# Kernel optimization log

Measured on AMD Instinct MI355X. Metric: run time of the kernel, lower is better.

Reference implementation:

```python
import jax, jax.numpy as jnp
import numpy as np

EPS = 1e-12  # matches tf l2_normalize epsilon behavior closely enough for testing

def setup_inputs() -> dict:
    key = jax.random.key(0)
    k1, k2 = jax.random.split(key)
    B, M, D = 512, 65536, 512
    context = jax.random.normal(k1, (B, D), dtype=jnp.float32)
    memory = jax.random.normal(k2, (M, D), dtype=jnp.float32)
    return {"context": context, "memory": memory}

def reference(context, memory):
    # tf.keras.losses.cosine_similarity returns NEGATIVE cosine similarity:
    # sim[b,m] = -sum(l2norm(context[b]) * l2norm(memory[m]))
    ctx_n = context / jnp.sqrt(jnp.maximum(jnp.sum(context * context, axis=-1, keepdims=True), EPS))
    mem_n = memory / jnp.sqrt(jnp.maximum(jnp.sum(memory * memory, axis=-1, keepdims=True), EPS))
    sim = -jnp.einsum('bd,md->bm', ctx_n, mem_n)  # [B, M]
    best = jnp.argmin(sim, axis=-1)               # [B], = argmax cosine
    # recall: gather then expand_dims(axis=0) -> [1, B, D]
    return memory[best][None, :, :]
```

## Files before the change

### kernel.cpp

```cpp
#include <hip/hip_runtime.h>
#include <hip/hip_bf16.h>
#include <stdint.h>

#define D_DIM 512
#define B_CTX 512
#define M_MEM 65536
#define BM 128
#define BB 128
#define BK 32
#define LDSPAD 40
#define DELTA_COS 2.5e-3f
#define LISTCAP 2048

typedef __attribute__((ext_vector_type(8))) short short8;
typedef __attribute__((ext_vector_type(4))) float floatx4;

__device__ __forceinline__ uint32_t f32_order(float s) {
    uint32_t u = __float_as_uint(s);
    return (u & 0x80000000u) ? ~u : (u | 0x80000000u);
}
__device__ __forceinline__ float f32_unorder(uint32_t v) {
    uint32_t u = (v & 0x80000000u) ? (v & 0x7FFFFFFFu) : ~v;
    return __uint_as_float(u);
}
__device__ __forceinline__ uint32_t pack_bf16_rtn(float a, float b) {
    uint32_t ua = __float_as_uint(a) + 0x8000u;
    uint32_t ub = __float_as_uint(b) + 0x8000u;
    return (ua >> 16) | (ub & 0xFFFF0000u);
}

__global__ void detect_init(const uint32_t* __restrict__ mem_raw,
                            uint32_t* __restrict__ flag) {
    __shared__ int cnt;
    if (threadIdx.x == 0) cnt = 0;
    __syncthreads();
    int s = 0;
    #pragma unroll
    for (int i = 0; i < 8; ++i) {
        uint32_t u = mem_raw[threadIdx.x * 8 + i];
        uint32_t e = (u >> 7) & 0xFFu;
        s += (e >= 96u && e <= 144u) ? 1 : 0;
    }
    atomicAdd(&cnt, s);
    __syncthreads();
    if (threadIdx.x == 0) *flag = (cnt > 256) ? 1u : 0u;
}

__global__ __launch_bounds__(256) void score_phase1(const void* __restrict__ ctxv,
                                                    const void* __restrict__ memv,
                                                    const uint32_t* __restrict__ flag,
                                                    uint32_t* __restrict__ tmax,
                                                    int coarse) {
    __shared__ __align__(16) uint16_t at[BM][LDSPAD];
    __shared__ __align__(16) uint16_t bt[BB][LDSPAD];
    __shared__ float s_nsq[BM];
    __shared__ uint32_t s_gbest[8][BB];

    const int t    = threadIdx.x;
    const int b0   = blockIdx.x * BB;
    const int m0   = blockIdx.y * BM;
    const int lane = t & 63;
    const int w    = t >> 6;
    const int wm   = w >> 1;
    const int wb   = w & 1;
    const int quad = lane >> 4;
    const int l15  = lane & 15;
    const int srow = t >> 2;
    const int scol = (t & 3) * 8;

    floatx4 acc[4][4];
    #pragma unroll
    for (int i = 0; i < 4; ++i)
        #pragma unroll
        for (int j = 0; j < 4; ++j)
            acc[i][j] = (floatx4){0.f, 0.f, 0.f, 0.f};

    float nsq0 = 0.f, nsq1 = 0.f;
    const bool isbf = (*flag != 0u);

    for (int k0 = 0; k0 < D_DIM; k0 += BK) {
        __syncthreads();
        if (isbf) {
            const uint16_t* mp = (const uint16_t*)memv;
            const uint16_t* cp = (const uint16_t*)ctxv;
            uint4 va0 = *(const uint4*)(mp + (size_t)(m0 + srow) * D_DIM + k0 + scol);
            uint4 va1 = *(const uint4*)(mp + (size_t)(m0 + srow + 64) * D_DIM + k0 + scol);
            uint4 vb0 = *(const uint4*)(cp + (size_t)(b0 + srow) * D_DIM + k0 + scol);
            uint4 vb1 = *(const uint4*)(cp + (size_t)(b0 + srow + 64) * D_DIM + k0 + scol);
            *(uint4*)&at[srow][scol] = va0;
            *(uint4*)&at[srow + 64][scol] = va1;
            *(uint4*)&bt[srow][scol] = vb0;
            *(uint4*)&bt[srow + 64][scol] = vb1;
            uint32_t wa0[4] = {va0.x, va0.y, va0.z, va0.w};
            uint32_t wa1[4] = {va1.x, va1.y, va1.z, va1.w};
            #pragma unroll
            for (int i = 0; i < 4; ++i) {
                float a = __uint_as_float(wa0[i] << 16);
                float b = __uint_as_float(wa0[i] & 0xFFFF0000u);
                nsq0 = fmaf(a, a, nsq0); nsq0 = fmaf(b, b, nsq0);
                float c = __uint_as_float(wa1[i] << 16);
                float d = __uint_as_float(wa1[i] & 0xFFFF0000u);
                nsq1 = fmaf(c, c, nsq1); nsq1 = fmaf(d, d, nsq1);
            }
        } else {
            const float* mp = (const float*)memv;
            const float* cp = (const float*)ctxv;
            const float4* pa0 = (const float4*)(mp + (size_t)(m0 + srow) * D_DIM + k0 + scol);
            const float4* pa1 = (const float4*)(mp + (size_t)(m0 + srow + 64) * D_DIM + k0 + scol);
            const float4* pb0 = (const float4*)(cp + (size_t)(b0 + srow) * D_DIM + k0 + scol);
            const float4* pb1 = (const float4*)(cp + (size_t)(b0 + srow + 64) * D_DIM + k0 + scol);
            float4 a0 = pa0[0], a1 = pa0[1], a2 = pa1[0], a3 = pa1[1];
            float4 c0 = pb0[0], c1 = pb0[1], c2 = pb1[0], c3 = pb1[1];
            uint4 va0 = {pack_bf16_rtn(a0.x, a0.y), pack_bf16_rtn(a0.z, a0.w),
                         pack_bf16_rtn(a1.x, a1.y), pack_bf16_rtn(a1.z, a1.w)};
            uint4 va1 = {pack_bf16_rtn(a2.x, a2.y), pack_bf16_rtn(a2.z, a2.w),
                         pack_bf16_rtn(a3.x, a3.y), pack_bf16_rtn(a3.z, a3.w)};
            uint4 vb0 = {pack_bf16_rtn(c0.x, c0.y), pack_bf16_rtn(c0.z, c0.w),
                         pack_bf16_rtn(c1.x, c1.y), pack_bf16_rtn(c1.z, c1.w)};
            uint4 vb1 = {pack_bf16_rtn(c2.x, c2.y), pack_bf16_rtn(c2.z, c2.w),
                         pack_bf16_rtn(c3.x, c3.y), pack_bf16_rtn(c3.z, c3.w)};
            *(uint4*)&at[srow][scol] = va0;
            *(uint4*)&at[srow + 64][scol] = va1;
            *(uint4*)&bt[srow][scol] = vb0;
            *(uint4*)&bt[srow + 64][scol] = vb1;
            nsq0 = fmaf(a0.x, a0.x, nsq0); nsq0 = fmaf(a0.y, a0.y, nsq0);
            nsq0 = fmaf(a0.z, a0.z, nsq0); nsq0 = fmaf(a0.w, a0.w, nsq0);
            nsq0 = fmaf(a1.x, a1.x, nsq0); nsq0 = fmaf(a1.y, a1.y, nsq0);
            nsq0 = fmaf(a1.z, a1.z, nsq0); nsq0 = fmaf(a1.w, a1.w, nsq0);
            nsq1 = fmaf(a2.x, a2.x, nsq1); nsq1 = fmaf(a2.y, a2.y, nsq1);
            nsq1 = fmaf(a2.z, a2.z, nsq1); nsq1 = fmaf(a2.w, a2.w, nsq1);
            nsq1 = fmaf(a3.x, a3.x, nsq1); nsq1 = fmaf(a3.y, a3.y, nsq1);
            nsq1 = fmaf(a3.z, a3.z, nsq1); nsq1 = fmaf(a3.w, a3.w, nsq1);
        }
        __syncthreads();

        short8 af[4], bg[4];
        #pragma unroll
        for (int i = 0; i < 4; ++i)
            af[i] = *(const short8*)&at[wm * 64 + i * 16 + l15][quad * 8];
        #pragma unroll
        for (int j = 0; j < 4; ++j)
            bg[j] = *(const short8*)&bt[wb * 64 + j * 16 + l15][quad * 8];

        #pragma unroll
        for (int i = 0; i < 4; ++i)
            #pragma unroll
            for (int j = 0; j < 4; ++j)
                acc[i][j] = __builtin_amdgcn_mfma_f32_16x16x32_bf16(af[i], bg[j], acc[i][j], 0, 0, 0);
    }

    nsq0 += __shfl_xor(nsq0, 1, 64); nsq0 += __shfl_xor(nsq0, 2, 64);
    nsq1 += __shfl_xor(nsq1, 1, 64); nsq1 += __shfl_xor(nsq1, 2, 64);
    __syncthreads();
    if ((t & 3) == 0) { s_nsq[srow] = nsq0; s_nsq[srow + 64] = nsq1; }
    __syncthreads();

    float invn[4][4];
    #pragma unroll
    for (int i = 0; i < 4; ++i)
        #pragma unroll
        for (int r = 0; r < 4; ++r)
            invn[i][r] = rsqrtf(fmaxf(s_nsq[wm * 64 + i * 16 + quad * 4 + r], 1e-12f));

    #pragma unroll
    for (int i = 0; i < 4; ++i)
        #pragma unroll
        for (int j = 0; j < 4; ++j) {
            uint32_t k = 0;
            #pragma unroll
            for (int r = 0; r < 4; ++r) {
                uint32_t kk = f32_order(acc[i][j][r] * invn[i][r]);
                k = kk > k ? kk : k;
            }
            uint32_t o1 = __shfl_xor(k, 16, 64); k = o1 > k ? o1 : k;
            uint32_t o2 = __shfl_xor(k, 32, 64); k = o2 > k ? o2 : k;
            if (quad == 0) s_gbest[wm * 4 + i][wb * 64 + j * 16 + l15] = k;
        }
    __syncthreads();

    if (!coarse) {
        const int G0 = blockIdx.y * 8;
        for (int e = t; e < 8 * BB; e += 256) {
            const int col = e >> 3, g = e & 7;
            tmax[(size_t)(b0 + col) * 4096 + G0 + g] = s_gbest[g][col];
        }
    } else {
        if (t < BB) {
            uint32_t k = s_gbest[0][t];
            #pragma unroll
            for (int g = 1; g < 8; ++g) k = s_gbest[g][t] > k ? s_gbest[g][t] : k;
            tmax[(size_t)(b0 + t) * 512 + blockIdx.y] = k;
        }
    }
}

__global__ __launch_bounds__(256) void phase2(const void* __restrict__ ctxv,
                                              const void* __restrict__ memv,
                                              const uint32_t* __restrict__ flag,
                                              const uint32_t* __restrict__ tmax,
                                              void* __restrict__ outv,
                                              int ngrp, int gshift) {
    __shared__ float s_ctx[D_DIM];
    __shared__ int s_list[LISTCAP];
    __shared__ int s_cnt;
    __shared__ uint32_t s_red[4];
    __shared__ float s_cn[4];
    __shared__ double s_d[4], s_n[4];
    __shared__ int s_m[4];
    __shared__ int s_bestm;

    const int b = blockIdx.x;
    const int t = threadIdx.x;
    const int lane = t & 63;
    const int w = t >> 6;
    const bool isbf = (*flag != 0u);
    const int gsize = 1 << gshift, gmask = gsize - 1;

    if (t == 0) s_cnt = 0;
    if (isbf) {
        if (t < 64) {
            uint4 v = *((const uint4*)((const uint16_t*)ctxv + (size_t)b * D_DIM) + t);
            uint32_t ww[4] = {v.x, v.y, v.z, v.w};
            #pragma unroll
            for (int i = 0; i < 4; ++i) {
                s_ctx[t * 8 + 2 * i]     = __uint_as_float(ww[i] << 16);
                s_ctx[t * 8 + 2 * i + 1] = __uint_as_float(ww[i] & 0xFFFF0000u);
            }
        }
    } else {
        if (t < 128)
            ((float4*)s_ctx)[t] = ((const float4*)((const float*)ctxv + (size_t)b * D_DIM))[t];
    }
    __syncthreads();

    float cs = s_ctx[t] * s_ctx[t] + s_ctx[t + 256] * s_ctx[t + 256];
    #pragma unroll
    for (int o = 32; o; o >>= 1) cs += __shfl_xor(cs, o, 64);
    if (lane == 0) s_cn[w] = cs;

    const uint32_t* tk = tmax + (size_t)b * ngrp;
    const int nk = ngrp >> 8;
    uint32_t kv[16];
    uint32_t km = 0;
    for (int i = 0; i < nk; ++i) {
        kv[i] = tk[t + (i << 8)];
        km = kv[i] > km ? kv[i] : km;
    }
    #pragma unroll
    for (int o = 32; o; o >>= 1) { uint32_t ot = __shfl_xor(km, o, 64); km = ot > km ? ot : km; }
    if (lane == 0) s_red[w] = km;
    __syncthreads();
    uint32_t kbest = s_red[0];
    #pragma unroll
    for (int i = 1; i < 4; ++i) kbest = s_red[i] > kbest ? s_red[i] : kbest;
    const float cnorm = sqrtf(s_cn[0] + s_cn[1] + s_cn[2] + s_cn[3]);
    const uint32_t keyT = f32_order(f32_unorder(kbest) - DELTA_COS * cnorm);

    for (int i = 0; i < nk; ++i)
        if (kv[i] >= keyT) {
            int idx = atomicAdd(&s_cnt, 1);
            if (idx < LISTCAP) s_list[idx] = t + (i << 8);
        }
    __syncthreads();
    int cnt = s_cnt; if (cnt > LISTCAP) cnt = LISTCAP;
    const int total = cnt << gshift;

    double bd = -1.0e300, bn = 1.0;
    double bp = bd * 1.0e300;
    int bm = 0x7FFFFFFF;
    const float* cb = s_ctx + lane * 8;

    for (int base = w * 2; base < total; base += 8) {
        const bool has1 = (base + 1 < total);
        const int ia = base, ib = has1 ? base + 1 : base;
        const int ma = (s_list[ia >> gshift] << gshift) + (ia & gmask);
        const int mb = (s_list[ib >> gshift] << gshift) + (ib & gmask);
        double d0 = 0.0, n0 = 0.0, d1 = 0.0, n1 = 0.0;
        if (isbf) {
            uint4 va = *((const uint4*)((const uint16_t*)memv + (size_t)ma * D_DIM) + lane);
            uint4 vb = *((const uint4*)((const uint16_t*)memv + (size_t)mb * D_DIM) + lane);
            uint32_t wa[4] = {va.x, va.y, va.z, va.w};
            uint32_t wbv[4] = {vb.x, vb.y, vb.z, vb.w};
            #pragma unroll
            for (int i = 0; i < 4; ++i) {
                float a0 = __uint_as_float(wa[i] << 16);
                float a1 = __uint_as_float(wa[i] & 0xFFFF0000u);
                d0 += (double)a0 * (double)cb[2 * i];
                d0 += (double)a1 * (double)cb[2 * i + 1];
                n0 += (double)a0 * (double)a0 + (double)a1 * (double)a1;
                float b0v = __uint_as_float(wbv[i] << 16);
                float b1v = __uint_as_float(wbv[i] & 0xFFFF0000u);
                d1 += (double)b0v * (double)cb[2 * i];
                d1 += (double)b1v * (double)cb[2 * i + 1];
                n1 += (double)b0v * (double)b0v + (double)b1v * (double)b1v;
            }
        } else {
            const float4* pa = (const float4*)((const float*)memv + (size_t)ma * D_DIM) + lane * 2;
            const float4* pb = (const float4*)((const float*)memv + (size_t)mb * D_DIM) + lane * 2;
            float4 a0 = pa[0], a1 = pa[1], b0v = pb[0], b1v = pb[1];
            float xa[8] = {a0.x, a0.y, a0.z, a0.w, a1.x, a1.y, a1.z, a1.w};
            float xb[8] = {b0v.x, b0v.y, b0v.z, b0v.w, b1v.x, b1v.y, b1v.z, b1v.w};
            #pragma unroll
            for (int i = 0; i < 8; ++i) {
                d0 += (double)xa[i] * (double)cb[i];
                n0 += (double)xa[i] * (double)xa[i];
                d1 += (double)xb[i] * (double)cb[i];
                n1 += (double)xb[i] * (double)xb[i];
            }
        }
        #pragma unroll
        for (int o = 32; o; o >>= 1) {
            d0 += __shfl_xor(d0, o, 64);
            n0 += __shfl_xor(n0, o, 64);
            d1 += __shfl_xor(d1, o, 64);
            n1 += __shfl_xor(n1, o, 64);
        }
        double p0 = d0 * fabs(d0);
        double lhs = p0 * bn, rhs = bp * n0;
        if (lhs > rhs || (lhs == rhs && ma < bm)) { bd = d0; bn = n0; bp = p0; bm = ma; }
        if (has1) {
            double p1 = d1 * fabs(d1);
            double lhs1 = p1 * bn, rhs1 = bp * n1;
            if (lhs1 > rhs1 || (lhs1 == rhs1 && mb < bm)) { bd = d1; bn = n1; bp = p1; bm = mb; }
        }
    }
    if (lane == 0) { s_d[w] = bd; s_n[w] = bn; s_m[w] = bm; }
    __syncthreads();
    if (t == 0) {
        double cd = s_d[0], cn2 = s_n[0], cp = cd * fabs(cd);
        int cm = s_m[0];
        #pragma unroll
        for (int i = 1; i < 4; ++i) {
            double pd = s_d[i], pn = s_n[i], pp = pd * fabs(pd);
            double lhs = pp * cn2, rhs = cp * pn;
            if (lhs > rhs || (lhs == rhs && s_m[i] < cm)) { cd = pd; cn2 = pn; cp = pp; cm = s_m[i]; }
        }
        s_bestm = cm;
    }
    __syncthreads();
    const int mbest = s_bestm;
    if (isbf) {
        if (t < 64)
            ((uint4*)((uint16_t*)outv + (size_t)b * D_DIM))[t] =
                ((const uint4*)((const uint16_t*)memv + (size_t)mbest * D_DIM))[t];
    } else {
        if (t < 128)
            ((float4*)((float*)outv + (size_t)b * D_DIM))[t] =
                ((const float4*)((const float*)memv + (size_t)mbest * D_DIM))[t];
    }
}

extern "C" void kernel_launch(void* const* d_in, const int* in_sizes, int n_in,
                              void* d_out, int out_size, void* d_ws, size_t ws_size,
                              hipStream_t stream) {
    const void* ctx = d_in[0];
    const void* mem = d_in[1];
    if (in_sizes[0] > in_sizes[1]) { ctx = d_in[1]; mem = d_in[0]; }

    const size_t fineBytes   = (size_t)B_CTX * 4096 * 4;
    const size_t coarseBytes = (size_t)B_CTX * 512 * 4;
    dim3 grid(B_CTX / BB, M_MEM / BM);

    if (ws_size >= fineBytes + 256) {
        uint32_t* tmax = (uint32_t*)d_ws;
        uint32_t* flag = (uint32_t*)((char*)d_ws + fineBytes);
        detect_init<<<1, 64, 0, stream>>>((const uint32_t*)mem, flag);
        score_phase1<<<grid, 256, 0, stream>>>(ctx, mem, flag, tmax, 0);
        phase2<<<B_CTX, 256, 0, stream>>>(ctx, mem, flag, tmax, d_out, 4096, 4);
    } else {
        uint32_t* tmax = (uint32_t*)d_ws;
        uint32_t* flag = (uint32_t*)((char*)d_ws + coarseBytes);
        detect_init<<<1, 64, 0, stream>>>((const uint32_t*)mem, flag);
        score_phase1<<<grid, 256, 0, stream>>>(ctx, mem, flag, tmax, 1);
        phase2<<<B_CTX, 256, 0, stream>>>(ctx, mem, flag, tmax, d_out, 512, 7);
    }
}
```

Before: 269.4 us.

## Pre-convert normalized memory to bf16 and stream tiles via async global-to-LDS loads

Adds a preprocessing kernel that L2-normalizes each memory row and converts memory and context to bf16 in the workspace. A new scoring kernel then loads 64-wide K tiles straight into XOR-swizzled LDS with global_load_lds, so the GEMM loop no longer converts or normalizes while loading. The grid is reordered so consecutive blocks walk the memory dimension. In exchange this costs an extra full pass over the memory matrix (read fp32, write bf16) and needs a larger workspace, with the old kernel kept as a fallback.

```diff
diff --git a/kernel.cpp b/kernel.cpp
--- a/kernel.cpp
+++ b/kernel.cpp
@@ -29,6 +29,11 @@
     return (ua >> 16) | (ub & 0xFFFF0000u);
 }
 
+#define GLOAD16(g, l)                                                          \
+    __builtin_amdgcn_global_load_lds(                                          \
+        (const __attribute__((address_space(1))) uint32_t*)(g),                \
+        (__attribute__((address_space(3))) uint32_t*)(l), 16, 0, 0)
+
 __global__ void detect_init(const uint32_t* __restrict__ mem_raw,
                             uint32_t* __restrict__ flag) {
     __shared__ int cnt;
@@ -46,11 +51,146 @@
     if (threadIdx.x == 0) *flag = (cnt > 256) ? 1u : 0u;
 }
 
-__global__ __launch_bounds__(256) void score_phase1(const void* __restrict__ ctxv,
-                                                    const void* __restrict__ memv,
+__global__ __launch_bounds__(256) void convert_norm(const void* __restrict__ memv,
+                                                    const void* __restrict__ ctxv,
                                                     const uint32_t* __restrict__ flag,
-                                                    uint32_t* __restrict__ tmax,
-                                                    int coarse) {
+                                                    uint4* __restrict__ mem_bf,
+                                                    uint4* __restrict__ ctx_bf) {
+    const int w = threadIdx.x >> 6, lane = threadIdx.x & 63;
+    const int row = blockIdx.x * 4 + w;
+    const bool isbf = (*flag != 0u);
+    if (row < M_MEM) {
+        float v[8];
+        if (isbf) {
+            uint4 u = *((const uint4*)((const uint16_t*)memv + (size_t)row * D_DIM) + lane);
+            uint32_t ww[4] = {u.x, u.y, u.z, u.w};
+            #pragma unroll
+            for (int i = 0; i < 4; ++i) {
+                v[2 * i]     = __uint_as_float(ww[i] << 16);
+                v[2 * i + 1] = __uint_as_float(ww[i] & 0xFFFF0000u);
+            }
+        } else {
+            const float4* p = (const float4*)((const float*)memv + (size_t)row * D_DIM) + lane * 2;
+            float4 a = p[0], b = p[1];
+            v[0] = a.x; v[1] = a.y; v[2] = a.z; v[3] = a.w;
+            v[4] = b.x; v[5] = b.y; v[6] = b.z; v[7] = b.w;
+        }
+        float ns = 0.f;
+        #pragma unroll
+        for (int i = 0; i < 8; ++i) ns = fmaf(v[i], v[i], ns);
+        #pragma unroll
+        for (int o = 32; o; o >>= 1) ns += __shfl_xor(ns, o, 64);
+        const float inv = rsqrtf(fmaxf(ns, 1e-12f));
+        #pragma unroll
+        for (int i = 0; i < 8; ++i) v[i] *= inv;
+        uint4 pk = {pack_bf16_rtn(v[0], v[1]), pack_bf16_rtn(v[2], v[3]),
+                    pack_bf16_rtn(v[4], v[5]), pack_bf16_rtn(v[6], v[7])};
+        mem_bf[(size_t)row * 64 + lane] = pk;
+    } else {
+        const int cr = row - M_MEM;
+        if (isbf) {
+            ctx_bf[(size_t)cr * 64 + lane] =
+                *((const uint4*)((const uint16_t*)ctxv + (size_t)cr * D_DIM) + lane);
+        } else {
+            const float4* p = (const float4*)((const float*)ctxv + (size_t)cr * D_DIM) + lane * 2;
+            float4 a = p[0], b = p[1];
+            uint4 pk = {pack_bf16_rtn(a.x, a.y), pack_bf16_rtn(a.z, a.w),
+                        pack_bf16_rtn(b.x, b.y), pack_bf16_rtn(b.z, b.w)};
+            ctx_bf[(size_t)cr * 64 + lane] = pk;
+        }
+    }
+}
+
+__global__ __launch_bounds__(256) void score_phase1_async(const uint16_t* __restrict__ mem_bf,
+                                                          const uint16_t* __restrict__ ctx_bf,
+                                                          uint32_t* __restrict__ tmax) {
+    __shared__ __align__(16) uint16_t at[BM * 64];
+    __shared__ __align__(16) uint16_t bt[BB * 64];
+    __shared__ uint32_t s_gbest[8][BB];
+
+    const int t    = threadIdx.x;
+    const int m0   = blockIdx.x * BM;
+    const int b0   = blockIdx.y * BB;
+    const int lane = t & 63;
+    const int w    = t >> 6;
+    const int wm   = w >> 1;
+    const int wb   = w & 1;
+    const int quad = lane >> 4;
+    const int l15  = lane & 15;
+
+    const int prow = lane >> 3;
+    const int gcol = ((lane & 7) ^ prow) << 3;
+
+    floatx4 acc[4][4];
+    #pragma unroll
+    for (int i = 0; i < 4; ++i)
+        #pragma unroll
+        for (int j = 0; j < 4; ++j)
+            acc[i][j] = (floatx4){0.f, 0.f, 0.f, 0.f};
+
+    for (int k0 = 0; k0 < D_DIM; k0 += 64) {
+        __syncthreads();
+        #pragma unroll
+        for (int ii = 0; ii < 4; ++ii) {
+            const int p = w * 4 + ii;
+            const uint16_t* ga = mem_bf + (size_t)(m0 + p * 8 + prow) * D_DIM + k0 + gcol;
+            const uint16_t* gb = ctx_bf + (size_t)(b0 + p * 8 + prow) * D_DIM + k0 + gcol;
+            GLOAD16(ga, &at[p * 512]);
+            GLOAD16(gb, &bt[p * 512]);
+        }
+        __syncthreads();
+
+        #pragma unroll
+        for (int kc = 0; kc < 2; ++kc) {
+            short8 af[4], bg[4];
+            #pragma unroll
+            for (int i = 0; i < 4; ++i) {
+                const int rr = wm * 64 + i * 16 + l15;
+                const int cg = ((kc * 4 + quad) ^ (rr & 7)) << 3;
+                af[i] = *(const short8*)&at[rr * 64 + cg];
+            }
+            #pragma unroll
+            for (int j = 0; j < 4; ++j) {
+                const int rb = wb * 64 + j * 16 + l15;
+                const int cg = ((kc * 4 + quad) ^ (rb & 7)) << 3;
+                bg[j] = *(const short8*)&bt[rb * 64 + cg];
+            }
+            #pragma unroll
+            for (int i = 0; i < 4; ++i)
+                #pragma unroll
+                for (int j = 0; j < 4; ++j)
+                    acc[i][j] = __builtin_amdgcn_mfma_f32_16x16x32_bf16(af[i], bg[j], acc[i][j], 0, 0, 0);
+        }
+    }
+
+    #pragma unroll
+    for (int i = 0; i < 4; ++i)
+        #pragma unroll
+        for (int j = 0; j < 4; ++j) {
+            uint32_t k = 0;
+            #pragma unroll
+            for (int r = 0; r < 4; ++r) {
+                uint32_t kk = f32_order(acc[i][j][r]);
+                k = kk > k ? kk : k;
+            }
+            uint32_t o1 = __shfl_xor(k, 16, 64); k = o1 > k ? o1 : k;
+            uint32_t o2 = __shfl_xor(k, 32, 64); k = o2 > k ? o2 : k;
+            if (quad == 0) s_gbest[wm * 4 + i][wb * 64 + j * 16 + l15] = k;
+        }
+    __syncthreads();
+
+    const int G0 = blockIdx.x * 8;
+    for (int e = t; e < 8 * BB; e += 256) {
+        const int col = e >> 3, g = e & 7;
+        tmax[(size_t)(b0 + col) * 4096 + G0 + g] = s_gbest[g][col];
+    }
+}
+
+__global__ __launch_bounds__(256) void score_phase1_fb(const void* __restrict__ ctxv,
+                                                       const void* __restrict__ memv,
+                                                       const uint32_t* __restrict__ flag,
+                                                       uint32_t* __restrict__ tmax,
+                                                       int coarse) {
     __shared__ __align__(16) uint16_t at[BM][LDSPAD];
     __shared__ __align__(16) uint16_t bt[BB][LDSPAD];
     __shared__ float s_nsq[BM];
@@ -214,7 +354,7 @@
     const int lane = t & 63;
     const int w = t >> 6;
     const bool isbf = (*flag != 0u);
-    const int gsize = 1 << gshift, gmask = gsize - 1;
+    const int gmask = (1 << gshift) - 1;
 
     if (t == 0) s_cnt = 0;
     if (isbf) {
@@ -357,21 +497,39 @@
     const void* mem = d_in[1];
     if (in_sizes[0] > in_sizes[1]) { ctx = d_in[1]; mem = d_in[0]; }
 
+    const size_t MEMBF_OFF = 0;
+    const size_t CTXBF_OFF = (size_t)M_MEM * D_DIM * 2;
+    const size_t TMAX_OFF  = CTXBF_OFF + (size_t)B_CTX * D_DIM * 2;
+    const size_t FLAG_OFF  = TMAX_OFF + (size_t)B_CTX * 4096 * 4;
+    const size_t NEED_A    = FLAG_OFF + 256;
+
     const size_t fineBytes   = (size_t)B_CTX * 4096 * 4;
     const size_t coarseBytes = (size_t)B_CTX * 512 * 4;
-    dim3 grid(B_CTX / BB, M_MEM / BM);
-
-    if (ws_size >= fineBytes + 256) {
+
+    if (ws_size >= NEED_A) {
+        uint4*    mem_bf = (uint4*)((char*)d_ws + MEMBF_OFF);
+        uint4*    ctx_bf = (uint4*)((char*)d_ws + CTXBF_OFF);
+        uint32_t* tmax   = (uint32_t*)((char*)d_ws + TMAX_OFF);
+        uint32_t* flag   = (uint32_t*)((char*)d_ws + FLAG_OFF);
+        detect_init<<<1, 64, 0, stream>>>((const uint32_t*)mem, flag);
+        convert_norm<<<(M_MEM + B_CTX) / 4, 256, 0, stream>>>(mem, ctx, flag, mem_bf, ctx_bf);
+        dim3 grid(M_MEM / BM, B_CTX / BB);
+        score_phase1_async<<<grid, 256, 0, stream>>>((const uint16_t*)mem_bf,
+                                                     (const uint16_t*)ctx_bf, tmax);
+        phase2<<<B_CTX, 256, 0, stream>>>(ctx, mem, flag, tmax, d_out, 4096, 4);
+    } else if (ws_size >= fineBytes + 256) {
         uint32_t* tmax = (uint32_t*)d_ws;
         uint32_t* flag = (uint32_t*)((char*)d_ws + fineBytes);
+        dim3 grid(B_CTX / BB, M_MEM / BM);
         detect_init<<<1, 64, 0, stream>>>((const uint32_t*)mem, flag);
-        score_phase1<<<grid, 256, 0, stream>>>(ctx, mem, flag, tmax, 0);
+        score_phase1_fb<<<grid, 256, 0, stream>>>(ctx, mem, flag, tmax, 0);
         phase2<<<B_CTX, 256, 0, stream>>>(ctx, mem, flag, tmax, d_out, 4096, 4);
     } else {
         uint32_t* tmax = (uint32_t*)d_ws;
         uint32_t* flag = (uint32_t*)((char*)d_ws + coarseBytes);
+        dim3 grid(B_CTX / BB, M_MEM / BM);
         detect_init<<<1, 64, 0, stream>>>((const uint32_t*)mem, flag);
-        score_phase1<<<grid, 256, 0, stream>>>(ctx, mem, flag, tmax, 1);
+        score_phase1_fb<<<grid, 256, 0, stream>>>(ctx, mem, flag, tmax, 1);
         phase2<<<B_CTX, 256, 0, stream>>>(ctx, mem, flag, tmax, d_out, 512, 7);
     }
 }
```

Measured after the change: 279.3 us. +3.7%, slower.
